# Kernel optimization log

Hardware: AMD Instinct MI355X
Metric: run time of the kernel (lower is better)

The kernel has to match this reference:

```python
import jax, jax.numpy as jnp
import numpy as np

N_NODES = 100000
N_EDGES = 500000
B = 256
NUM_RELS = 200
VEC = 300   # rel_vectors.shape[1]
D = 32      # rel_emb_dim
MODES = 6


def setup_inputs() -> dict:
    key = jax.random.key(0)
    ks = jax.random.split(key, 16)
    s = 0.05
    return {
        'edge_src': jax.random.randint(ks[0], (N_EDGES,), 0, N_NODES, dtype=jnp.int32),
        'edge_dst': jax.random.randint(ks[1], (N_EDGES,), 0, N_NODES, dtype=jnp.int32),
        'edge_type': jax.random.randint(ks[2], (N_EDGES,), 0, NUM_RELS, dtype=jnp.int32),
        'head_ids': jnp.arange(B, dtype=jnp.int32),            # one head node per subgraph
        'tail_ids': jnp.arange(B, dtype=jnp.int32) + B,        # one tail node per subgraph (disjoint)
        'rel_labels': jax.random.randint(ks[3], (B,), 0, NUM_RELS, dtype=jnp.int32),
        'rel_vectors': jax.random.normal(ks[4], (NUM_RELS, VEC), jnp.float32),
        'W1': jax.random.normal(ks[5], (VEC, D), jnp.float32) * s,
        'b1': jax.random.normal(ks[6], (D,), jnp.float32) * s,
        'W2': jax.random.normal(ks[7], (D, D), jnp.float32) * s,
        'b2': jax.random.normal(ks[8], (D,), jnp.float32) * s,
        'reld_W': jax.random.normal(ks[9], (MODES, D, D), jnp.float32) * s,
        'reld_b': jax.random.normal(ks[10], (MODES, D), jnp.float32) * s,
        'conc_W': jax.random.normal(ks[11], (2 * D, D), jnp.float32) * s,
        'conc_b': jax.random.normal(ks[12], (D,), jnp.float32) * s,
        'fc_W': jax.random.normal(ks[13], (D, 1), jnp.float32) * s,
        'fc_b': jax.random.normal(ks[14], (1,), jnp.float32) * s,
    }


def _mode_segments(edge_src, edge_dst, head_ids, tail_ids):
    """Per-edge segment id (batch index, or B=dropped) for each of the 6 modes.
    Equivalent to the torch sparse mask build: mode5 = out_edge_out*in_edge_in,
    mode6 = in_edge_out*out_edge_in, modes 1-4 with overlaps subtracted out."""
    b = head_ids.shape[0]
    bidx = jnp.arange(b, dtype=jnp.int32)
    head_batch = jnp.full((N_NODES,), -1, jnp.int32).at[head_ids].set(bidx)
    tail_batch = jnp.full((N_NODES,), -1, jnp.int32).at[tail_ids].set(bidx)
    hb_s = head_batch[edge_src]
    hb_d = head_batch[edge_dst]
    tb_s = tail_batch[edge_src]
    tb_d = tail_batch[edge_dst]
    m5 = (hb_s >= 0) & (hb_s == tb_d)   # src==head_b and dst==tail_b
    m6 = (hb_d >= 0) & (hb_d == tb_s)   # dst==head_b and src==tail_b
    drop = jnp.int32(b)
    return [
        jnp.where((hb_d >= 0) & ~m6, hb_d, drop),  # in_edge_out  - mode6
        jnp.where((hb_s >= 0) & ~m5, hb_s, drop),  # out_edge_out - mode5
        jnp.where((tb_d >= 0) & ~m5, tb_d, drop),  # in_edge_in   - mode5
        jnp.where((tb_s >= 0) & ~m6, tb_s, drop),  # out_edge_in  - mode6
        jnp.where(m5, hb_s, drop),                 # mode5
        jnp.where(m6, hb_d, drop),                 # mode6
    ]


def reference(edge_src, edge_dst, edge_type, head_ids, tail_ids, rel_labels,
              rel_vectors, W1, b1, W2, b2, reld_W, reld_b, conc_W, conc_b, fc_W, fc_b):
    b = head_ids.shape[0]
    segs = _mode_segments(edge_src, edge_dst, head_ids, tail_ids)

    # edge embeddings: rel_vectors[type] -> transform1 -> transform2   [E, D]
    e = rel_vectors[edge_type] @ W1 + b1
    e = e @ W2 + b2
    # per-mode fc_reld transforms: [MODES, E, D]
    Y = jnp.einsum('ed,mdk->mek', e, reld_W) + reld_b[:, None, :]

    ones_e = jnp.ones(edge_src.shape, e.dtype)
    acc = jnp.zeros((b, Y.shape[-1]), e.dtype)
    for i in range(MODES):
        agg = jax.ops.segment_sum(Y[i], segs[i], num_segments=b + 1)[:b]
        cnt = jax.ops.segment_sum(ones_e, segs[i], num_segments=b + 1)[:b]
        acc = acc + agg / (cnt[:, None] + 1e-30)
    rel_neighbor = acc / MODES

    r = rel_vectors[rel_labels] @ W1 + b1
    r = r @ W2 + b2

    h = jnp.concatenate([rel_neighbor, r], axis=-1) @ conc_W + conc_b
    h = jax.nn.relu(h)
    # F.normalize(p=2, dim=-1)
    g_rep = h / jnp.maximum(jnp.linalg.norm(h, axis=-1, keepdims=True), 1e-12)
    return g_rep @ fc_W + fc_b  # [B, 1]
```

## Files before the change

### kernel.cpp

```cpp
#include <hip/hip_runtime.h>
#include <hip/hip_bf16.h>

constexpr int N_NODES  = 100000;
constexpr int BATCH    = 256;
constexpr int NUM_RELS = 200;
constexpr int VEC      = 300;
constexpr int DIM      = 32;
constexpr int MODES    = 6;

constexpr int BLOCK        = 256;
constexpr int BM_WORDS     = (N_NODES + 31) / 32;
constexpr int RELS_PER_BLK = 8;
constexpr int NRB          = NUM_RELS / RELS_PER_BLK;
static_assert(NUM_RELS % RELS_PER_BLK == 0, "rel blocks assume exact tiling");
constexpr int EDGE_BLKS    = 256;
constexpr int CAP          = 64;
constexpr int HASHN        = 1024;
constexpr unsigned HEMPTY  = 0xFFFFFFFFu;
constexpr int MAXM         = 512;
constexpr int NPROD        = NRB + EDGE_BLKS;

__device__ __forceinline__ void st_agent(float* p, float v) {
    __hip_atomic_store(p, v, __ATOMIC_RELAXED, __HIP_MEMORY_SCOPE_AGENT);
}
__device__ __forceinline__ void st_agent(unsigned* p, unsigned v) {
    __hip_atomic_store(p, v, __ATOMIC_RELAXED, __HIP_MEMORY_SCOPE_AGENT);
}
__device__ __forceinline__ float ld_agent_f(const float* p) {
    return __hip_atomic_load(p, __ATOMIC_RELAXED, __HIP_MEMORY_SCOPE_AGENT);
}
__device__ __forceinline__ unsigned ld_agent_u(const unsigned* p) {
    return __hip_atomic_load(p, __ATOMIC_RELAXED, __HIP_MEMORY_SCOPE_AGENT);
}

template <typename T> __device__ __forceinline__ float ldf(const void* p, int i);
template <> __device__ __forceinline__ float ldf<float>(const void* p, int i) {
    return ((const float*)p)[i];
}
template <> __device__ __forceinline__ float ldf<__hip_bfloat16>(const void* p, int i) {
    return __bfloat162float(((const __hip_bfloat16*)p)[i]);
}

__device__ __forceinline__ void detect_dtype(const void* rel_vectors, int* sflag) {
    const int tid = threadIdx.x;
    if (tid < 64) {
        unsigned short p = ((const unsigned short*)rel_vectors)[tid];
        unsigned long long mk = __ballot(((p >> 7) & 0xFF) > 140);
        if (tid == 0) *sflag = (mk == 0ull);
    }
    __syncthreads();
}

__device__ __forceinline__ void hinsert(unsigned* hkey, unsigned* hval, int node, unsigned v) {
    unsigned h = ((unsigned)node * 2654435761u) >> 22;
    for (;;) {
        unsigned prev = atomicCAS(&hkey[h], HEMPTY, (unsigned)node);
        if (prev == HEMPTY || prev == (unsigned)node) { atomicOr(&hval[h], v); return; }
        h = (h + 1) & (HASHN - 1);
    }
}
__device__ __forceinline__ unsigned hlookup(const unsigned* hkey, const unsigned* hval, int node) {
    unsigned h = ((unsigned)node * 2654435761u) >> 22;
    for (;;) {
        const unsigned k = hkey[h];
        if (k == (unsigned)node) return hval[h];
        if (k == HEMPTY) return 0u;
        h = (h + 1) & (HASHN - 1);
    }
}

template <typename T>
__device__ __forceinline__ void rel_body(const void* rel_vectors, const void* W1, const void* b1,
                                         const void* W2, const void* b2,
                                         const void* reld_W, const void* reld_b,
                                         float* E_rel, float* Y_rel,
                                         float (*rv)[VEC], float (*e1)[DIM], float (*e2)[DIM],
                                         int r0) {
    const int tid = threadIdx.x;
    const int g = tid >> 5, d = tid & 31;
    const int r = r0 + g;
    for (int v = d; v < VEC; v += 32) rv[g][v] = ldf<T>(rel_vectors, r * VEC + v);
    __syncthreads();
    float acc = ldf<T>(b1, d);
    for (int v = 0; v < VEC; ++v) acc += rv[g][v] * ldf<T>(W1, v * DIM + d);
    e1[g][d] = acc;
    __syncthreads();
    float a2 = ldf<T>(b2, d);
    for (int k = 0; k < DIM; ++k) a2 += e1[g][k] * ldf<T>(W2, k * DIM + d);
    e2[g][d] = a2;
    st_agent(&E_rel[r * DIM + d], a2);
    __syncthreads();
    for (int m = 0; m < MODES; ++m) {
        float y = ldf<T>(reld_b, m * DIM + d);
        for (int k = 0; k < DIM; ++k) y += e2[g][k] * ldf<T>(reld_W, (m * DIM + k) * DIM + d);
        st_agent(&Y_rel[(m * NUM_RELS + r) * DIM + d], y);
    }
}

template <typename T>
__device__ __forceinline__ void epilogue_math(const float* cat,
                                              const void* conc_W, const void* conc_b,
                                              const void* fc_W, const void* fc_b,
                                              void* out, int b) {
    const int tid = threadIdx.x;
    if (tid < DIM) {
        float h = ldf<T>(conc_b, tid);
        for (int k = 0; k < 2 * DIM; ++k) h += cat[k] * ldf<T>(conc_W, k * DIM + tid);
        h = fmaxf(h, 0.f);
        float n2 = h * h;
        #pragma unroll
        for (int off = 16; off >= 1; off >>= 1) n2 += __shfl_xor(n2, off);
        const float g = h / fmaxf(sqrtf(n2), 1e-12f);
        float pr = g * ldf<T>(fc_W, tid);
        #pragma unroll
        for (int off = 16; off >= 1; off >>= 1) pr += __shfl_xor(pr, off);
        if (tid == 0) {
            const float o = pr + ldf<T>(fc_b, 0);
            if constexpr (sizeof(T) == 2) ((__hip_bfloat16*)out)[b] = __float2bfloat16(o);
            else                          ((float*)out)[b] = o;
        }
    }
}

struct EdgeSmem {
    unsigned bm[BM_WORDS];
    unsigned hkey[HASHN];
    unsigned hval[HASHN];
    unsigned obuf[CAP];
    int ocnt;
};
struct RelSmem {
    float rv[RELS_PER_BLK][VEC];
    float e1[RELS_PER_BLK][DIM];
    float e2[RELS_PER_BLK][DIM];
    int sflag;
};
struct FinSmem {
    float    accf[MODES][DIM];
    float    totf[MODES];
    unsigned mbuf[MAXM];
    int      mcnt;
    float    cat[2 * DIM];
    int      sflag;
};

__global__ __launch_bounds__(BLOCK) void k_fused(
        const int* __restrict__ edge_src, const int* __restrict__ edge_dst,
        const int* __restrict__ edge_type,
        const int* __restrict__ head_ids, const int* __restrict__ tail_ids,
        const int* __restrict__ rel_labels,
        const void* rel_vectors, const void* W1, const void* b1,
        const void* W2, const void* b2, const void* reld_W, const void* reld_b,
        const void* conc_W, const void* conc_b, const void* fc_W, const void* fc_b,
        unsigned* list, unsigned* listcnt, float* E_rel, float* Y_rel,
        int* done, void* out, int n_edges) {
    union SmemU { RelSmem rel; EdgeSmem edge; FinSmem fin; };
    __shared__ SmemU s;
    const int bid = blockIdx.x, tid = threadIdx.x;

    if (bid < NRB) {
        detect_dtype(rel_vectors, &s.rel.sflag);
        const int r0 = bid * RELS_PER_BLK;
        if (s.rel.sflag)
            rel_body<__hip_bfloat16>(rel_vectors, W1, b1, W2, b2, reld_W, reld_b,
                                     E_rel, Y_rel, s.rel.rv, s.rel.e1, s.rel.e2, r0);
        else
            rel_body<float>(rel_vectors, W1, b1, W2, b2, reld_W, reld_b,
                            E_rel, Y_rel, s.rel.rv, s.rel.e1, s.rel.e2, r0);
        asm volatile("s_waitcnt vmcnt(0)" ::: "memory");
        __syncthreads();
        if (tid == 0)
            __hip_atomic_fetch_add(done, 1, __ATOMIC_RELAXED, __HIP_MEMORY_SCOPE_AGENT);
        return;
    }

    const int eb = bid - NRB;
    for (int i = tid; i < BM_WORDS; i += BLOCK) s.edge.bm[i] = 0u;
    for (int i = tid; i < HASHN; i += BLOCK) { s.edge.hkey[i] = HEMPTY; s.edge.hval[i] = 0u; }
    if (tid == 0) s.edge.ocnt = 0;
    __syncthreads();
    if (tid < BATCH) {
        const int h = head_ids[tid], t = tail_ids[tid];
        atomicOr(&s.edge.bm[h >> 5], 1u << (h & 31));
        atomicOr(&s.edge.bm[t >> 5], 1u << (t & 31));
        hinsert(s.edge.hkey, s.edge.hval, h, (unsigned)(tid + 1));
        hinsert(s.edge.hkey, s.edge.hval, t, (unsigned)(tid + 1) << 16);
    }
    __syncthreads();

    auto emit = [&](unsigned code) {
        const int idx = atomicAdd(&s.edge.ocnt, 1);
        if (idx < CAP) s.edge.obuf[idx] = code;
    };
    auto classify = [&](int sn, int dn, unsigned bs, unsigned bd, int e) {
        const int t = edge_type[e];
        const unsigned ps = bs ? hlookup(s.edge.hkey, s.edge.hval, sn) : 0u;
        const unsigned pd = bd ? hlookup(s.edge.hkey, s.edge.hval, dn) : 0u;
        const int hbs = (int)(ps & 0xFFFFu) - 1, tbs = (int)(ps >> 16) - 1;
        const int hbd = (int)(pd & 0xFFFFu) - 1, tbd = (int)(pd >> 16) - 1;
        const bool m5 = (hbs >= 0) && (hbs == tbd);
        const bool m6 = (hbd >= 0) && (hbd == tbs);
        if (hbd >= 0)        emit(((m6 ? 5u : 0u) * BATCH + hbd) * NUM_RELS + t);
        if (hbs >= 0)        emit(((m5 ? 4u : 1u) * BATCH + hbs) * NUM_RELS + t);
        if (tbd >= 0 && !m5) emit((2u * BATCH + tbd) * NUM_RELS + t);
        if (tbs >= 0 && !m6) emit((3u * BATCH + tbs) * NUM_RELS + t);
    };

    const int n4 = n_edges >> 2;
    const int sstr = EDGE_BLKS * BLOCK;
    const int et = eb * BLOCK + tid;
    const int4* src4 = (const int4*)edge_src;
    const int4* dst4 = (const int4*)edge_dst;
    for (int i = et; i < n4; i += sstr) {
        const int4 s4 = src4[i];
        const int4 d4 = dst4[i];
        #pragma unroll
        for (int j = 0; j < 4; ++j) {
            const int sn = (&s4.x)[j];
            const int dn = (&d4.x)[j];
            const unsigned bs = (s.edge.bm[sn >> 5] >> (sn & 31)) & 1u;
            const unsigned bd = (s.edge.bm[dn >> 5] >> (dn & 31)) & 1u;
            if (!(bs | bd)) continue;
            classify(sn, dn, bs, bd, i * 4 + j);
        }
    }
    const int rem = n_edges & 3;
    if (et < rem) {
        const int e = n4 * 4 + et;
        const int sn = edge_src[e], dn = edge_dst[e];
        const unsigned bs = (s.edge.bm[sn >> 5] >> (sn & 31)) & 1u;
        const unsigned bd = (s.edge.bm[dn >> 5] >> (dn & 31)) & 1u;
        if (bs | bd) classify(sn, dn, bs, bd, e);
    }
    __syncthreads();
    const int oc = min(s.edge.ocnt, CAP);
    if (tid == 0) st_agent(&listcnt[eb], (unsigned)oc);
    for (int i = tid; i < oc; i += BLOCK) st_agent(&list[i * EDGE_BLKS + eb], s.edge.obuf[i]);

    asm volatile("s_waitcnt vmcnt(0)" ::: "memory");
    __syncthreads();
    if (tid == 0) {
        __hip_atomic_fetch_add(done, 1, __ATOMIC_RELAXED, __HIP_MEMORY_SCOPE_AGENT);
        while (__hip_atomic_fetch_add(done, 0, __ATOMIC_RELAXED,
                                      __HIP_MEMORY_SCOPE_AGENT) < NPROD)
            __builtin_amdgcn_s_sleep(8);
    }
    __syncthreads();

    const int b = eb;
    for (int i = tid; i < MODES * DIM; i += BLOCK) ((float*)s.fin.accf)[i] = 0.f;
    if (tid < MODES) s.fin.totf[tid] = 0.f;
    if (tid == 0) s.fin.mcnt = 0;
    const int c = (int)ld_agent_u(&listcnt[tid]);
    detect_dtype(rel_vectors, &s.fin.sflag);

    for (int i = 0; i < c; ++i) {
        const unsigned code = ld_agent_u(&list[i * EDGE_BLKS + tid]);
        const int bb = (int)((code / NUM_RELS) % BATCH);
        if (bb == b) {
            const int k = atomicAdd(&s.fin.mcnt, 1);
            if (k < MAXM) s.fin.mbuf[k] = code;
        }
    }
    __syncthreads();

    const int mc = min(s.fin.mcnt, MAXM);
    const int d = tid & 31;
    for (int j = tid >> 5; j < mc; j += 8) {
        const unsigned code = s.fin.mbuf[j];
        const int m = (int)(code / (NUM_RELS * BATCH));
        const int t = (int)(code % NUM_RELS);
        atomicAdd(&s.fin.accf[m][d], ld_agent_f(&Y_rel[(m * NUM_RELS + t) * DIM + d]));
        if (d == 0) atomicAdd(&s.fin.totf[m], 1.f);
    }
    __syncthreads();

    if (tid < DIM) {
        float rn = 0.f;
        for (int m = 0; m < MODES; ++m) rn += s.fin.accf[m][tid] / (s.fin.totf[m] + 1e-30f);
        s.fin.cat[tid] = rn / (float)MODES;
        s.fin.cat[DIM + tid] = ld_agent_f(&E_rel[rel_labels[b] * DIM + tid]);
    }
    __syncthreads();
    if (s.fin.sflag) epilogue_math<__hip_bfloat16>(s.fin.cat, conc_W, conc_b, fc_W, fc_b, out, b);
    else             epilogue_math<float>(s.fin.cat, conc_W, conc_b, fc_W, fc_b, out, b);
}

extern "C" void kernel_launch(void* const* d_in, const int* in_sizes, int n_in,
                              void* d_out, int out_size, void* d_ws, size_t ws_size,
                              hipStream_t stream) {
    const int* edge_src   = (const int*)d_in[0];
    const int* edge_dst   = (const int*)d_in[1];
    const int* edge_type  = (const int*)d_in[2];
    const int* head_ids   = (const int*)d_in[3];
    const int* tail_ids   = (const int*)d_in[4];
    const int* rel_labels = (const int*)d_in[5];
    const void* rel_vectors = d_in[6];
    const void* W1     = d_in[7];
    const void* b1     = d_in[8];
    const void* W2     = d_in[9];
    const void* b2     = d_in[10];
    const void* reld_W = d_in[11];
    const void* reld_b = d_in[12];
    const void* conc_W = d_in[13];
    const void* conc_b = d_in[14];
    const void* fc_W   = d_in[15];
    const void* fc_b   = d_in[16];

    const int n_edges = in_sizes[0];

    unsigned* list    = (unsigned*)d_ws;
    unsigned* listcnt = list + EDGE_BLKS * CAP;
    float*    E_rel   = (float*)(listcnt + EDGE_BLKS);
    float*    Y_rel   = E_rel + NUM_RELS * DIM;
    int*      done    = (int*)(Y_rel + MODES * NUM_RELS * DIM);

    hipMemsetAsync(done, 0, sizeof(int), stream);
    k_fused<<<NRB + EDGE_BLKS, BLOCK, 0, stream>>>(
        edge_src, edge_dst, edge_type, head_ids, tail_ids, rel_labels,
        rel_vectors, W1, b1, W2, b2, reld_W, reld_b,
        conc_W, conc_b, fc_W, fc_b,
        list, listcnt, E_rel, Y_rel, done, d_out, n_edges);
}
```

Baseline: 124.4 us.

## Scatter classified edge codes directly into global per-batch buckets

Edge blocks now append each classified code straight into a per-batch global bucket through agent-scope atomics, instead of staging codes in a per-block shared buffer and publishing a list. After the grid barrier, each finisher block reads only its own bucket, so it no longer scans every block's list (256 lists read by each of 256 blocks). Zero-init work is also moved ahead of the spin-wait so it overlaps. The cost is global atomics per emitted code, plus a fixed per-batch capacity of 128 that silently drops extra entries.

```diff
diff --git a/kernel.cpp b/kernel.cpp
--- a/kernel.cpp
+++ b/kernel.cpp
@@ -14,11 +14,10 @@
 constexpr int NRB          = NUM_RELS / RELS_PER_BLK;
 static_assert(NUM_RELS % RELS_PER_BLK == 0, "rel blocks assume exact tiling");
 constexpr int EDGE_BLKS    = 256;
-constexpr int CAP          = 64;
 constexpr int HASHN        = 1024;
 constexpr unsigned HEMPTY  = 0xFFFFFFFFu;
-constexpr int MAXM         = 512;
-constexpr int NPROD        = NRB + EDGE_BLKS;
+constexpr int MAXB         = 128;
+constexpr unsigned NPROD   = NRB + EDGE_BLKS;
 
 __device__ __forceinline__ void st_agent(float* p, float v) {
     __hip_atomic_store(p, v, __ATOMIC_RELAXED, __HIP_MEMORY_SCOPE_AGENT);
@@ -126,8 +125,6 @@
     unsigned bm[BM_WORDS];
     unsigned hkey[HASHN];
     unsigned hval[HASHN];
-    unsigned obuf[CAP];
-    int ocnt;
 };
 struct RelSmem {
     float rv[RELS_PER_BLK][VEC];
@@ -138,8 +135,7 @@
 struct FinSmem {
     float    accf[MODES][DIM];
     float    totf[MODES];
-    unsigned mbuf[MAXM];
-    int      mcnt;
+    unsigned mbuf[MAXB];
     float    cat[2 * DIM];
     int      sflag;
 };
@@ -152,8 +148,8 @@
         const void* rel_vectors, const void* W1, const void* b1,
         const void* W2, const void* b2, const void* reld_W, const void* reld_b,
         const void* conc_W, const void* conc_b, const void* fc_W, const void* fc_b,
-        unsigned* list, unsigned* listcnt, float* E_rel, float* Y_rel,
-        int* done, void* out, int n_edges) {
+        unsigned* bucket, unsigned* bcnt, float* E_rel, float* Y_rel,
+        unsigned* done, void* out, int n_edges) {
     union SmemU { RelSmem rel; EdgeSmem edge; FinSmem fin; };
     __shared__ SmemU s;
     const int bid = blockIdx.x, tid = threadIdx.x;
@@ -170,14 +166,13 @@
         asm volatile("s_waitcnt vmcnt(0)" ::: "memory");
         __syncthreads();
         if (tid == 0)
-            __hip_atomic_fetch_add(done, 1, __ATOMIC_RELAXED, __HIP_MEMORY_SCOPE_AGENT);
+            __hip_atomic_fetch_add(done, 1u, __ATOMIC_RELAXED, __HIP_MEMORY_SCOPE_AGENT);
         return;
     }
 
     const int eb = bid - NRB;
     for (int i = tid; i < BM_WORDS; i += BLOCK) s.edge.bm[i] = 0u;
     for (int i = tid; i < HASHN; i += BLOCK) { s.edge.hkey[i] = HEMPTY; s.edge.hval[i] = 0u; }
-    if (tid == 0) s.edge.ocnt = 0;
     __syncthreads();
     if (tid < BATCH) {
         const int h = head_ids[tid], t = tail_ids[tid];
@@ -188,22 +183,23 @@
     }
     __syncthreads();
 
-    auto emit = [&](unsigned code) {
-        const int idx = atomicAdd(&s.edge.ocnt, 1);
-        if (idx < CAP) s.edge.obuf[idx] = code;
+    auto emit = [&](int bb, unsigned code) {
+        const unsigned idx = __hip_atomic_fetch_add(&bcnt[bb], 1u, __ATOMIC_RELAXED,
+                                                    __HIP_MEMORY_SCOPE_AGENT);
+        if (idx < (unsigned)MAXB) st_agent(&bucket[bb * MAXB + (int)idx], code);
     };
     auto classify = [&](int sn, int dn, unsigned bs, unsigned bd, int e) {
-        const int t = edge_type[e];
+        const unsigned t = (unsigned)edge_type[e];
         const unsigned ps = bs ? hlookup(s.edge.hkey, s.edge.hval, sn) : 0u;
         const unsigned pd = bd ? hlookup(s.edge.hkey, s.edge.hval, dn) : 0u;
         const int hbs = (int)(ps & 0xFFFFu) - 1, tbs = (int)(ps >> 16) - 1;
         const int hbd = (int)(pd & 0xFFFFu) - 1, tbd = (int)(pd >> 16) - 1;
         const bool m5 = (hbs >= 0) && (hbs == tbd);
         const bool m6 = (hbd >= 0) && (hbd == tbs);
-        if (hbd >= 0)        emit(((m6 ? 5u : 0u) * BATCH + hbd) * NUM_RELS + t);
-        if (hbs >= 0)        emit(((m5 ? 4u : 1u) * BATCH + hbs) * NUM_RELS + t);
-        if (tbd >= 0 && !m5) emit((2u * BATCH + tbd) * NUM_RELS + t);
-        if (tbs >= 0 && !m6) emit((3u * BATCH + tbs) * NUM_RELS + t);
+        if (hbd >= 0)        emit(hbd, (m6 ? 5u : 0u) * NUM_RELS + t);
+        if (hbs >= 0)        emit(hbs, (m5 ? 4u : 1u) * NUM_RELS + t);
+        if (tbd >= 0 && !m5) emit(tbd, 2u * NUM_RELS + t);
+        if (tbs >= 0 && !m6) emit(tbs, 3u * NUM_RELS + t);
     };
 
     const int n4 = n_edges >> 2;
@@ -232,43 +228,32 @@
         const unsigned bd = (s.edge.bm[dn >> 5] >> (dn & 31)) & 1u;
         if (bs | bd) classify(sn, dn, bs, bd, e);
     }
-    __syncthreads();
-    const int oc = min(s.edge.ocnt, CAP);
-    if (tid == 0) st_agent(&listcnt[eb], (unsigned)oc);
-    for (int i = tid; i < oc; i += BLOCK) st_agent(&list[i * EDGE_BLKS + eb], s.edge.obuf[i]);
 
     asm volatile("s_waitcnt vmcnt(0)" ::: "memory");
     __syncthreads();
-    if (tid == 0) {
-        __hip_atomic_fetch_add(done, 1, __ATOMIC_RELAXED, __HIP_MEMORY_SCOPE_AGENT);
-        while (__hip_atomic_fetch_add(done, 0, __ATOMIC_RELAXED,
-                                      __HIP_MEMORY_SCOPE_AGENT) < NPROD)
-            __builtin_amdgcn_s_sleep(8);
-    }
-    __syncthreads();
-
-    const int b = eb;
+    if (tid == 0)
+        __hip_atomic_fetch_add(done, 1u, __ATOMIC_RELAXED, __HIP_MEMORY_SCOPE_AGENT);
+
     for (int i = tid; i < MODES * DIM; i += BLOCK) ((float*)s.fin.accf)[i] = 0.f;
     if (tid < MODES) s.fin.totf[tid] = 0.f;
-    if (tid == 0) s.fin.mcnt = 0;
-    const int c = (int)ld_agent_u(&listcnt[tid]);
     detect_dtype(rel_vectors, &s.fin.sflag);
 
-    for (int i = 0; i < c; ++i) {
-        const unsigned code = ld_agent_u(&list[i * EDGE_BLKS + tid]);
-        const int bb = (int)((code / NUM_RELS) % BATCH);
-        if (bb == b) {
-            const int k = atomicAdd(&s.fin.mcnt, 1);
-            if (k < MAXM) s.fin.mbuf[k] = code;
-        }
-    }
-    __syncthreads();
-
-    const int mc = min(s.fin.mcnt, MAXM);
+    if (tid == 0) {
+        while (__hip_atomic_fetch_add(done, 0u, __ATOMIC_RELAXED,
+                                      __HIP_MEMORY_SCOPE_AGENT) < NPROD)
+            __builtin_amdgcn_s_sleep(16);
+    }
+    __syncthreads();
+
+    const int b = eb;
+    const int mc = min((int)ld_agent_u(&bcnt[b]), MAXB);
+    if (tid < mc) s.fin.mbuf[tid] = ld_agent_u(&bucket[b * MAXB + tid]);
+    __syncthreads();
+
     const int d = tid & 31;
     for (int j = tid >> 5; j < mc; j += 8) {
         const unsigned code = s.fin.mbuf[j];
-        const int m = (int)(code / (NUM_RELS * BATCH));
+        const int m = (int)(code / NUM_RELS);
         const int t = (int)(code % NUM_RELS);
         atomicAdd(&s.fin.accf[m][d], ld_agent_f(&Y_rel[(m * NUM_RELS + t) * DIM + d]));
         if (d == 0) atomicAdd(&s.fin.totf[m], 1.f);
@@ -309,16 +294,16 @@
 
     const int n_edges = in_sizes[0];
 
-    unsigned* list    = (unsigned*)d_ws;
-    unsigned* listcnt = list + EDGE_BLKS * CAP;
-    float*    E_rel   = (float*)(listcnt + EDGE_BLKS);
-    float*    Y_rel   = E_rel + NUM_RELS * DIM;
-    int*      done    = (int*)(Y_rel + MODES * NUM_RELS * DIM);
-
-    hipMemsetAsync(done, 0, sizeof(int), stream);
+    unsigned* bucket = (unsigned*)d_ws;
+    unsigned* bcnt   = bucket + BATCH * MAXB;
+    unsigned* done   = bcnt + BATCH;
+    float*    E_rel  = (float*)(done + 1);
+    float*    Y_rel  = E_rel + NUM_RELS * DIM;
+
+    hipMemsetAsync(bcnt, 0, (BATCH + 1) * sizeof(unsigned), stream);
     k_fused<<<NRB + EDGE_BLKS, BLOCK, 0, stream>>>(
         edge_src, edge_dst, edge_type, head_ids, tail_ids, rel_labels,
         rel_vectors, W1, b1, W2, b2, reld_W, reld_b,
         conc_W, conc_b, fc_W, fc_b,
-        list, listcnt, E_rel, Y_rel, done, d_out, n_edges);
-}
+        bucket, bcnt, E_rel, Y_rel, done, d_out, n_edges);
+}
```

Measured after the change: 118.8 us. -4.5%, faster.
